# Kernel tuning notes

Measured on AMD Instinct MI355X. Metric: run time of the kernel, lower is better.

## Reference

```python
import jax, jax.numpy as jnp
import numpy as np

B, S, D, H = 4, 2048, 512, 512

def setup_inputs() -> dict:
    key = jax.random.key(0)
    ks = jax.random.split(key, 9)
    sc_d = 1.0 / np.sqrt(D)
    sc_s = 1.0 / np.sqrt(S)
    return {
        "x": jax.random.normal(ks[0], (B, S, D), dtype=jnp.float32),
        "Wq": jax.random.normal(ks[1], (D, H), dtype=jnp.float32) * sc_d,
        "bq": jnp.zeros((H,), dtype=jnp.float32),
        "Wk": jax.random.normal(ks[2], (D, H), dtype=jnp.float32) * sc_d,
        "bk": jnp.zeros((H,), dtype=jnp.float32),
        "Wv": jax.random.normal(ks[3], (D, H), dtype=jnp.float32) * sc_d,
        "bv": jnp.zeros((H,), dtype=jnp.float32),
        "Wd": jax.random.normal(ks[4], (S, H), dtype=jnp.float32) * sc_s,
        "bd": jnp.zeros((H,), dtype=jnp.float32),
    }

def reference(x, Wq, bq, Wk, bk, Wv, bv, Wd, bd):
    # q, k, v: [B, S, H]
    q = x @ Wq + bq
    k = x @ Wk + bk
    v = x @ Wv + bv
    # raw scores: [B, S, S]
    qk = jnp.einsum('bsh,bth->bst', q, k)
    # Dense+sigmoid over the last (seqlen) axis: [B, S, H]
    dense_out = jax.nn.sigmoid(qk @ Wd + bd)
    # value weights: [B, S, S]
    vw = jnp.einsum('bsh,bth->bst', dense_out, v)
    # out: [B, S, D]
    return jnp.einsum('bst,btd->bsd', vw, x)
```

## Files before the change

kernel.cpp:

```cpp
#include <hip/hip_runtime.h>
#include <hip/hip_bf16.h>
#include <stdint.h>

#define BB 4
#define SS 2048
#define DD 512
#define HH 512

typedef __attribute__((ext_vector_type(8))) short short8;
typedef __attribute__((ext_vector_type(4))) float floatx4;

typedef __attribute__((address_space(3))) uint32_t lds_u32_t;
typedef const __attribute__((address_space(1))) uint32_t glb_u32_t;

__device__ __forceinline__ void gload_lds16(const void* g, void* l) {
  __builtin_amdgcn_global_load_lds((glb_u32_t*)g, (lds_u32_t*)l, 16, 0, 0);
}

__device__ __forceinline__ short f2bf(float f) {
  __hip_bfloat16 h = __float2bfloat16(f);
  return __builtin_bit_cast(short, h);
}

__device__ __forceinline__ float bf2f(short s) {
  uint32_t u = ((uint32_t)(uint16_t)s) << 16;
  return __builtin_bit_cast(float, u);
}

template <int BM>
__device__ __forceinline__ void gemm_mainloop(const short* __restrict__ Ab,
                                              const short* __restrict__ Bb,
                                              int lda, int ldb, int K,
                                              floatx4 (&acc)[BM / 32][4]) {
  constexpr int BK = 32;
  constexpr int MF = BM / 32;
  __shared__ short As[BM * BK];
  __shared__ short Bs[128 * BK];

  const int t = threadIdx.x;
  const int lane = t & 63;
  const int wid = t >> 6;
  const int wr = wid >> 1, wc = wid & 1;
  const int r16 = lane & 15;
  const int kc = (lane >> 4) * 8;

  const int st_row = t >> 2;
  const int st_k = (t & 3) * 8;

#pragma unroll
  for (int i = 0; i < MF; i++)
#pragma unroll
    for (int j = 0; j < 4; j++) acc[i][j] = (floatx4)0.f;

  for (int k0 = 0; k0 < K; k0 += BK) {
#pragma unroll
    for (int i = 0; i < BM / 64; i++)
      gload_lds16(Ab + (long)(i * 64 + st_row) * lda + k0 + st_k,
                  &As[(i * 64 + st_row) * BK + st_k]);
#pragma unroll
    for (int i = 0; i < 2; i++)
      gload_lds16(Bb + (long)(i * 64 + st_row) * ldb + k0 + st_k,
                  &Bs[(i * 64 + st_row) * BK + st_k]);
    __syncthreads();

    short8 af[MF], bfr[4];
#pragma unroll
    for (int i = 0; i < MF; i++)
      af[i] = *(const short8*)&As[(wr * (BM / 2) + i * 16 + r16) * BK + kc];
#pragma unroll
    for (int j = 0; j < 4; j++)
      bfr[j] = *(const short8*)&Bs[(wc * 64 + j * 16 + r16) * BK + kc];
#pragma unroll
    for (int i = 0; i < MF; i++)
#pragma unroll
      for (int j = 0; j < 4; j++)
        acc[i][j] = __builtin_amdgcn_mfma_f32_16x16x32_bf16(af[i], bfr[j],
                                                            acc[i][j], 0, 0, 0);
    __syncthreads();
  }
}

template <int BM, int EPI>
__device__ __forceinline__ void epilogue_std(floatx4 (&acc)[BM / 32][4],
                                             void* __restrict__ Cm, long c_base,
                                             const float* __restrict__ bias,
                                             int ldc, long row0, long col0) {
  const int lane = threadIdx.x & 63;
  const int wid = threadIdx.x >> 6;
  const int wr = wid >> 1, wc = wid & 1;
  const int r16 = lane & 15;
#pragma unroll
  for (int i = 0; i < BM / 32; i++) {
    const long rbase = row0 + wr * (BM / 2) + i * 16 + (lane >> 4) * 4;
#pragma unroll
    for (int j = 0; j < 4; j++) {
      const long col = col0 + wc * 64 + j * 16 + r16;
      float bv = 0.f;
      if (EPI == 2) bv = bias[col];
#pragma unroll
      for (int rg = 0; rg < 4; rg++) {
        float v = acc[i][j][rg];
        if (EPI == 2) v = 1.f / (1.f + __expf(-(v + bv)));
        const long idx = c_base + (rbase + rg) * ldc + col;
        if (EPI == 3)
          ((float*)Cm)[idx] = v;
        else
          ((__hip_bfloat16*)Cm)[idx] = __float2bfloat16(v);
      }
    }
  }
}

template <int BM, int EPI>
__global__ __launch_bounds__(256) void gemm_bt(
    const short* __restrict__ A, const short* __restrict__ Bm,
    void* __restrict__ Cm, const float* __restrict__ bias, int K, int lda,
    int ldb, int ldc, long sA, long sB, long sC) {
  const int bz = blockIdx.z;
  floatx4 acc[BM / 32][4];
  const long row0 = (long)blockIdx.x * BM, col0 = (long)blockIdx.y * 128;
  gemm_mainloop<BM>(A + bz * sA + row0 * lda, Bm + bz * sB + col0 * ldb, lda,
                    ldb, K, acc);
  epilogue_std<BM, EPI>(acc, Cm, bz * sC, bias, ldc, row0, col0);
}

__global__ __launch_bounds__(256) void gemm_qkv(
    const short* __restrict__ xb, const short* __restrict__ WT,
    const float* __restrict__ bcat, short* __restrict__ q,
    short* __restrict__ kT, short* __restrict__ vT) {
  floatx4 acc[4][4];
  const long row0 = (long)blockIdx.x * 128;
  const int y = blockIdx.y;
  gemm_mainloop<128>(xb + row0 * DD, WT + (long)y * 128 * DD, DD, DD, DD, acc);

  const int lane = threadIdx.x & 63;
  const int wid = threadIdx.x >> 6;
  const int wr = wid >> 1, wc = wid & 1;
  const int r16 = lane & 15;
  const int hi4 = (lane >> 4) * 4;
  const int mode = y >> 2;
  const int b = (int)(row0 >> 11);
  const int sblk = (int)(row0 & 2047);
  short* tp = (mode == 1) ? kT : vT;
#pragma unroll
  for (int i = 0; i < 4; i++) {
    const int s0 = sblk + wr * 64 + i * 16 + hi4;
#pragma unroll
    for (int j = 0; j < 4; j++) {
      const int colg = y * 128 + wc * 64 + j * 16 + r16;
      const float bv = bcat[colg];
      short o[4];
#pragma unroll
      for (int rg = 0; rg < 4; rg++) o[rg] = f2bf(acc[i][j][rg] + bv);
      if (mode == 0) {
#pragma unroll
        for (int rg = 0; rg < 4; rg++)
          q[((long)b * SS + s0 + rg) * HH + colg] = o[rg];
      } else {
        const int cl = colg - mode * 512;
        *(uint64_t*)&tp[((long)b * HH + cl) * SS + s0] = *(uint64_t*)o;
      }
    }
  }
}

__global__ __launch_bounds__(256) void gemm_dual_split(
    const short* __restrict__ WdT, const short* __restrict__ kT,
    short* __restrict__ partM2, const short* __restrict__ xT,
    const short* __restrict__ vT, short* __restrict__ partM3) {
  const int bz = blockIdx.z;
  const int tb = bz >> 2, sp = bz & 3;
  const int task = tb >> 2, b = tb & 3;
  const short* A = (task ? xT + (long)b * HH * SS : WdT) + sp * 512;
  const short* B = (task ? vT : kT) + (long)b * HH * SS + sp * 512;
  short* C = (task ? partM3 : partM2) + ((long)(tb & 3) * 4 + sp) * HH * HH;
  floatx4 acc[2][4];
  const long row0 = (long)blockIdx.x * 64, col0 = (long)blockIdx.y * 128;
  gemm_mainloop<64>(A + row0 * SS, B + col0 * SS, SS, SS, 512, acc);
  epilogue_std<64, 0>(acc, C, 0, nullptr, HH, row0, col0);
}

__global__ __launch_bounds__(256) void reduce_part(
    const short* __restrict__ partM2, const short* __restrict__ partM3,
    short* __restrict__ M2, short* __restrict__ M3t) {
  const int z = blockIdx.z;
  const int b = z & 3;
  const short* src = (z < 4 ? partM2 : partM3) + (long)b * 4 * HH * HH;
  short* dst = (z < 4 ? M2 : M3t) + (long)b * HH * HH;
  const long i = ((long)blockIdx.x * 256 + threadIdx.x) * 8;
  float s[8];
#pragma unroll
  for (int j = 0; j < 8; j++) s[j] = 0.f;
#pragma unroll
  for (int sp = 0; sp < 4; sp++) {
    short8 v = *(const short8*)&src[(long)sp * HH * HH + i];
#pragma unroll
    for (int j = 0; j < 8; j++) s[j] += bf2f(v[j]);
  }
  short o[8];
#pragma unroll
  for (int j = 0; j < 8; j++) o[j] = f2bf(s[j]);
  *(short8*)&dst[i] = *(short8*)o;
}

__global__ void tr_x(const float* __restrict__ x, short* __restrict__ xb,
                     short* __restrict__ xT) {
  __shared__ float tile[32][33];
  const long b = blockIdx.z;
  const float* in = x + b * SS * DD;
  const int c0 = blockIdx.x * 32, r0 = blockIdx.y * 32;
  const int tx = threadIdx.x, ty = threadIdx.y;
#pragma unroll
  for (int i = 0; i < 32; i += 8) {
    float v = in[(long)(r0 + ty + i) * DD + c0 + tx];
    tile[ty + i][tx] = v;
    xb[(b * SS + r0 + ty + i) * DD + c0 + tx] = f2bf(v);
  }
  __syncthreads();
#pragma unroll
  for (int i = 0; i < 32; i += 8)
    xT[(b * DD + c0 + ty + i) * SS + r0 + tx] = f2bf(tile[tx][ty + i]);
}

__global__ void prep_w(const float* __restrict__ Wq,
                       const float* __restrict__ Wk,
                       const float* __restrict__ Wv,
                       const float* __restrict__ Wd,
                       const float* __restrict__ bq,
                       const float* __restrict__ bk,
                       const float* __restrict__ bv, short* __restrict__ WT,
                       short* __restrict__ WdT, float* __restrict__ bcat) {
  __shared__ float tile[32][33];
  const int z = blockIdx.z, yb = blockIdx.y;
  const int tx = threadIdx.x, ty = threadIdx.y;
  if (z < 3) {
    if (yb < 16) {
      const float* in = z == 0 ? Wq : (z == 1 ? Wk : Wv);
      short* out = WT + (long)z * HH * DD;
      const int c0 = blockIdx.x * 32, r0 = yb * 32;
#pragma unroll
      for (int i = 0; i < 32; i += 8)
        tile[ty + i][tx] = in[(long)(r0 + ty + i) * HH + c0 + tx];
      __syncthreads();
#pragma unroll
      for (int i = 0; i < 32; i += 8)
        out[(long)(c0 + ty + i) * DD + r0 + tx] = f2bf(tile[tx][ty + i]);
    } else if (z == 0 && yb < 22 && blockIdx.x == 0) {
      const int i = (yb - 16) * 256 + ty * 32 + tx;
      bcat[i] = i < 512 ? bq[i] : (i < 1024 ? bk[i - 512] : bv[i - 1024]);
    }
  } else {
    const int c0 = blockIdx.x * 32, r0 = yb * 32;
#pragma unroll
    for (int i = 0; i < 32; i += 8)
      tile[ty + i][tx] = Wd[(long)(r0 + ty + i) * HH + c0 + tx];
    __syncthreads();
#pragma unroll
    for (int i = 0; i < 32; i += 8)
      WdT[(long)(c0 + ty + i) * SS + r0 + tx] = f2bf(tile[tx][ty + i]);
  }
}

extern "C" void kernel_launch(void* const* d_in, const int* in_sizes, int n_in,
                              void* d_out, int out_size, void* d_ws,
                              size_t ws_size, hipStream_t stream) {
  (void)in_sizes;
  (void)n_in;
  (void)out_size;
  (void)ws_size;
  const float* x = (const float*)d_in[0];
  const float* Wq = (const float*)d_in[1];
  const float* bq = (const float*)d_in[2];
  const float* Wk = (const float*)d_in[3];
  const float* bk = (const float*)d_in[4];
  const float* Wv = (const float*)d_in[5];
  const float* bv = (const float*)d_in[6];
  const float* Wd = (const float*)d_in[7];
  const float* bd = (const float*)d_in[8];

  char* w = (char*)d_ws;
  auto alloc = [&](size_t bytes) {
    char* p = w;
    w += (bytes + 255) & ~(size_t)255;
    return p;
  };
  short* xb = (short*)alloc((size_t)BB * SS * DD * 2);
  short* xT = (short*)alloc((size_t)BB * DD * SS * 2);
  short* WT = (short*)alloc((size_t)3 * HH * DD * 2);
  short* WdT = (short*)alloc((size_t)HH * SS * 2);
  float* bcat = (float*)alloc((size_t)3 * HH * 4);
  short* q = (short*)alloc((size_t)BB * SS * HH * 2);
  short* kT = (short*)alloc((size_t)BB * HH * SS * 2);
  short* vT = (short*)alloc((size_t)BB * HH * SS * 2);
  short* partM2 = (short*)alloc((size_t)BB * 4 * HH * HH * 2);
  short* partM3 = (short*)alloc((size_t)BB * 4 * HH * HH * 2);
  short* M2 = (short*)alloc((size_t)BB * HH * HH * 2);
  short* M3t = (short*)alloc((size_t)BB * DD * HH * 2);
  short* dense = (short*)alloc((size_t)BB * SS * HH * 2);

  dim3 tb(32, 8);
  tr_x<<<dim3(DD / 32, SS / 32, BB), tb, 0, stream>>>(x, xb, xT);
  prep_w<<<dim3(16, 64, 4), tb, 0, stream>>>(Wq, Wk, Wv, Wd, bq, bk, bv, WT,
                                             WdT, bcat);

  gemm_qkv<<<dim3(BB * SS / 128, 12, 1), 256, 0, stream>>>(xb, WT, bcat, q, kT,
                                                           vT);
  gemm_dual_split<<<dim3(8, 4, 32), 256, 0, stream>>>(WdT, kT, partM2, xT, vT,
                                                      partM3);
  reduce_part<<<dim3(128, 1, 8), 256, 0, stream>>>(partM2, partM3, M2, M3t);
  gemm_bt<64, 2><<<dim3(SS / 64, HH / 128, BB), 256, 0, stream>>>(
      q, M2, dense, bd, HH, HH, HH, HH, (long)SS * HH, (long)HH * HH,
      (long)SS * HH);
  gemm_bt<64, 3><<<dim3(SS / 64, DD / 128, BB), 256, 0, stream>>>(
      dense, M3t, d_out, nullptr, HH, HH, HH, DD, (long)SS * HH, (long)DD * HH,
      (long)SS * DD);
}
```

Measured before the change: 90.72 us.

## Double GEMM K-tile with XOR-swizzled LDS and merge prep kernels

The shared GEMM mainloop now stages a K-tile of 64 instead of 32, halving the number of barrier pairs per K. It XOR-swizzles the 16-byte chunks in LDS to avoid bank conflicts on the wider rows. It also merges the x transpose/convert kernel and the weight-prep kernel into a single launch to save one launch gap. Doubling LDS per block may reduce occupancy.

```diff
diff --git a/kernel.cpp b/kernel.cpp
--- a/kernel.cpp
+++ b/kernel.cpp
@@ -32,7 +32,7 @@
                                               const short* __restrict__ Bb,
                                               int lda, int ldb, int K,
                                               floatx4 (&acc)[BM / 32][4]) {
-  constexpr int BK = 32;
+  constexpr int BK = 64;
   constexpr int MF = BM / 32;
   __shared__ short As[BM * BK];
   __shared__ short Bs[128 * BK];
@@ -42,10 +42,10 @@
   const int wid = t >> 6;
   const int wr = wid >> 1, wc = wid & 1;
   const int r16 = lane & 15;
-  const int kc = (lane >> 4) * 8;
-
-  const int st_row = t >> 2;
-  const int st_k = (t & 3) * 8;
+  const int hi = lane >> 4;
+
+  const int srow = t >> 3;
+  const int schunk = t & 7;
 
 #pragma unroll
   for (int i = 0; i < MF; i++)
@@ -54,28 +54,45 @@
 
   for (int k0 = 0; k0 < K; k0 += BK) {
 #pragma unroll
-    for (int i = 0; i < BM / 64; i++)
-      gload_lds16(Ab + (long)(i * 64 + st_row) * lda + k0 + st_k,
-                  &As[(i * 64 + st_row) * BK + st_k]);
-#pragma unroll
-    for (int i = 0; i < 2; i++)
-      gload_lds16(Bb + (long)(i * 64 + st_row) * ldb + k0 + st_k,
-                  &Bs[(i * 64 + st_row) * BK + st_k]);
+    for (int s = 0; s < BM / 32; s++) {
+      const int row = s * 32 + srow;
+      const int g = schunk ^ (row & 7);
+      gload_lds16(Ab + (long)row * lda + k0 + g * 8,
+                  &As[row * BK + schunk * 8]);
+    }
+#pragma unroll
+    for (int s = 0; s < 4; s++) {
+      const int row = s * 32 + srow;
+      const int g = schunk ^ (row & 7);
+      gload_lds16(Bb + (long)row * ldb + k0 + g * 8,
+                  &Bs[row * BK + schunk * 8]);
+    }
     __syncthreads();
 
-    short8 af[MF], bfr[4];
+    short8 af[MF][2], bfr[4][2];
+#pragma unroll
+    for (int i = 0; i < MF; i++) {
+      const int row = wr * (BM / 2) + i * 16 + r16;
+      const int x7 = row & 7;
+      af[i][0] = *(const short8*)&As[row * BK + (hi ^ x7) * 8];
+      af[i][1] = *(const short8*)&As[row * BK + ((hi + 4) ^ x7) * 8];
+    }
+#pragma unroll
+    for (int j = 0; j < 4; j++) {
+      const int row = wc * 64 + j * 16 + r16;
+      const int x7 = row & 7;
+      bfr[j][0] = *(const short8*)&Bs[row * BK + (hi ^ x7) * 8];
+      bfr[j][1] = *(const short8*)&Bs[row * BK + ((hi + 4) ^ x7) * 8];
+    }
 #pragma unroll
     for (int i = 0; i < MF; i++)
-      af[i] = *(const short8*)&As[(wr * (BM / 2) + i * 16 + r16) * BK + kc];
-#pragma unroll
-    for (int j = 0; j < 4; j++)
-      bfr[j] = *(const short8*)&Bs[(wc * 64 + j * 16 + r16) * BK + kc];
-#pragma unroll
-    for (int i = 0; i < MF; i++)
-#pragma unroll
-      for (int j = 0; j < 4; j++)
-        acc[i][j] = __builtin_amdgcn_mfma_f32_16x16x32_bf16(af[i], bfr[j],
-                                                            acc[i][j], 0, 0, 0);
+#pragma unroll
+      for (int j = 0; j < 4; j++) {
+        acc[i][j] = __builtin_amdgcn_mfma_f32_16x16x32_bf16(
+            af[i][0], bfr[j][0], acc[i][j], 0, 0, 0);
+        acc[i][j] = __builtin_amdgcn_mfma_f32_16x16x32_bf16(
+            af[i][1], bfr[j][1], acc[i][j], 0, 0, 0);
+      }
     __syncthreads();
   }
 }
@@ -203,40 +220,35 @@
   *(short8*)&dst[i] = *(short8*)o;
 }
 
-__global__ void tr_x(const float* __restrict__ x, short* __restrict__ xb,
-                     short* __restrict__ xT) {
-  __shared__ float tile[32][33];
-  const long b = blockIdx.z;
-  const float* in = x + b * SS * DD;
-  const int c0 = blockIdx.x * 32, r0 = blockIdx.y * 32;
-  const int tx = threadIdx.x, ty = threadIdx.y;
-#pragma unroll
-  for (int i = 0; i < 32; i += 8) {
-    float v = in[(long)(r0 + ty + i) * DD + c0 + tx];
-    tile[ty + i][tx] = v;
-    xb[(b * SS + r0 + ty + i) * DD + c0 + tx] = f2bf(v);
-  }
-  __syncthreads();
-#pragma unroll
-  for (int i = 0; i < 32; i += 8)
-    xT[(b * DD + c0 + ty + i) * SS + r0 + tx] = f2bf(tile[tx][ty + i]);
-}
-
-__global__ void prep_w(const float* __restrict__ Wq,
-                       const float* __restrict__ Wk,
-                       const float* __restrict__ Wv,
-                       const float* __restrict__ Wd,
-                       const float* __restrict__ bq,
-                       const float* __restrict__ bk,
-                       const float* __restrict__ bv, short* __restrict__ WT,
-                       short* __restrict__ WdT, float* __restrict__ bcat) {
+__global__ void prep(const float* __restrict__ x, const float* __restrict__ Wq,
+                     const float* __restrict__ Wk, const float* __restrict__ Wv,
+                     const float* __restrict__ Wd, const float* __restrict__ bq,
+                     const float* __restrict__ bk, const float* __restrict__ bv,
+                     short* __restrict__ xb, short* __restrict__ xT,
+                     short* __restrict__ WT, short* __restrict__ WdT,
+                     float* __restrict__ bcat) {
   __shared__ float tile[32][33];
   const int z = blockIdx.z, yb = blockIdx.y;
   const int tx = threadIdx.x, ty = threadIdx.y;
-  if (z < 3) {
+  if (z < 4) {
+    const long b = z;
+    const float* in = x + b * SS * DD;
+    const int c0 = blockIdx.x * 32, r0 = yb * 32;
+#pragma unroll
+    for (int i = 0; i < 32; i += 8) {
+      float v = in[(long)(r0 + ty + i) * DD + c0 + tx];
+      tile[ty + i][tx] = v;
+      xb[(b * SS + r0 + ty + i) * DD + c0 + tx] = f2bf(v);
+    }
+    __syncthreads();
+#pragma unroll
+    for (int i = 0; i < 32; i += 8)
+      xT[(b * DD + c0 + ty + i) * SS + r0 + tx] = f2bf(tile[tx][ty + i]);
+  } else if (z < 7) {
+    const int w = z - 4;
     if (yb < 16) {
-      const float* in = z == 0 ? Wq : (z == 1 ? Wk : Wv);
-      short* out = WT + (long)z * HH * DD;
+      const float* in = w == 0 ? Wq : (w == 1 ? Wk : Wv);
+      short* out = WT + (long)w * HH * DD;
       const int c0 = blockIdx.x * 32, r0 = yb * 32;
 #pragma unroll
       for (int i = 0; i < 32; i += 8)
@@ -245,7 +257,7 @@
 #pragma unroll
       for (int i = 0; i < 32; i += 8)
         out[(long)(c0 + ty + i) * DD + r0 + tx] = f2bf(tile[tx][ty + i]);
-    } else if (z == 0 && yb < 22 && blockIdx.x == 0) {
+    } else if (w == 0 && yb < 22 && blockIdx.x == 0) {
       const int i = (yb - 16) * 256 + ty * 32 + tx;
       bcat[i] = i < 512 ? bq[i] : (i < 1024 ? bk[i - 512] : bv[i - 1024]);
     }
@@ -299,9 +311,8 @@
   short* dense = (short*)alloc((size_t)BB * SS * HH * 2);
 
   dim3 tb(32, 8);
-  tr_x<<<dim3(DD / 32, SS / 32, BB), tb, 0, stream>>>(x, xb, xT);
-  prep_w<<<dim3(16, 64, 4), tb, 0, stream>>>(Wq, Wk, Wv, Wd, bq, bk, bv, WT,
-                                             WdT, bcat);
+  prep<<<dim3(16, 64, 8), tb, 0, stream>>>(x, Wq, Wk, Wv, Wd, bq, bk, bv, xb,
+                                           xT, WT, WdT, bcat);
 
   gemm_qkv<<<dim3(BB * SS / 128, 12, 1), 256, 0, stream>>>(xb, WT, bcat, q, kT,
                                                            vT);
```

Result: faster. 81.87 us (median of 2 runs) (-9.8%).
